# Optimization experiments

Measured on AMD Instinct MI355X. Metric: run time of the kernel, lower is better.

The kernel has to match this reference:

```python
import jax, jax.numpy as jnp
import numpy as np

EPS = 1e-5

def _ln(x):
    # LayerNorm over last dim, no affine (torch F.layer_norm default weight/bias None here)
    mu = jnp.mean(x, axis=-1, keepdims=True)
    var = jnp.var(x, axis=-1, keepdims=True)
    return (x - mu) * jax.lax.rsqrt(var + EPS)

def setup_inputs() -> dict:
    key = jax.random.key(0)
    B, S, IN, OUT = 4, 512, 256, 256
    HID = int(0.125 * IN)  # 32
    ks = jax.random.split(key, 9)
    s_in = 1.0 / np.sqrt(IN)
    s_hid = 1.0 / np.sqrt(HID)
    return {
        "x": jax.random.normal(ks[0], (B, S, IN), dtype=jnp.float32),
        # w_linear: Linear(IN->HID) then Linear(HID->IN*OUT)
        "w1": jax.random.uniform(ks[1], (HID, IN), jnp.float32, -s_in, s_in),
        "b1": jax.random.uniform(ks[2], (HID,), jnp.float32, -s_in, s_in),
        "w2": jax.random.uniform(ks[3], (IN * OUT, HID), jnp.float32, -s_hid, s_hid),
        "b2": jax.random.uniform(ks[4], (IN * OUT,), jnp.float32, -s_hid, s_hid),
        # b_linear: Linear(IN->HID) then Linear(HID->OUT)
        "u1": jax.random.uniform(ks[5], (HID, IN), jnp.float32, -s_in, s_in),
        "c1": jax.random.uniform(ks[6], (HID,), jnp.float32, -s_in, s_in),
        "u2": jax.random.uniform(ks[7], (OUT, HID), jnp.float32, -s_hid, s_hid),
        "c2": jax.random.uniform(ks[8], (OUT,), jnp.float32, -s_hid, s_hid),
    }

def reference(x, w1, b1, w2, b2, u1, c1, u2, c2):
    B, S, IN = x.shape
    OUT = u2.shape[0]
    # weight generation: [B,S,IN] -> [B,S,HID] -> [B,S,OUT*IN]
    hw = jnp.einsum('bsi,hi->bsh', x, w1) + b1
    w = jnp.einsum('bsh,oh->bso', hw, w2) + b2  # o = OUT*IN flattened
    w = w.reshape(B, S, OUT, IN)
    w = _ln(w)  # LayerNorm over IN
    # bias generation: [B,S,IN] -> [B,S,HID] -> [B,S,OUT]
    hb = jnp.einsum('bsi,hi->bsh', x, u1) + c1
    b = jnp.einsum('bsh,oh->bso', hb, u2) + c2
    b = _ln(b)  # LayerNorm over OUT
    # batched matvec: y[b,s,o] = sum_i w[b,s,o,i] * x[b,s,i] + b[b,s,o]
    y = jnp.einsum('bsoi,bsi->bso', w, x) + b
    return y
```

## Files before the change

### kernel.cpp

```cpp
#include <hip/hip_runtime.h>
#include <hip/hip_bf16.h>
#include <stdint.h>

#define EPS 1e-5f

typedef __attribute__((ext_vector_type(8))) short short8;
typedef __attribute__((ext_vector_type(4))) float f32x4;

typedef const __attribute__((address_space(1))) uint32_t gas_u32;
typedef __attribute__((address_space(3))) uint32_t las_u32;

static __device__ __forceinline__ void gll16(const void* src, void* dst) {
    __builtin_amdgcn_global_load_lds((gas_u32*)src, (las_u32*)dst, 16, 0, 0);
}
static __device__ __forceinline__ unsigned short f2b(float f) {
    __hip_bfloat16 h = __float2bfloat16(f);
    return *reinterpret_cast<unsigned short*>(&h);
}
static __device__ __forceinline__ float b2f(unsigned short u) {
    union { unsigned int i; float f; } x; x.i = ((unsigned int)u) << 16; return x.f;
}
static __device__ __forceinline__ unsigned int pk2(float a, float b) {
    return (unsigned int)f2b(a) | ((unsigned int)f2b(b) << 16);
}

__device__ void prep_body(int o, const float* __restrict__ w2,
                          const float* __restrict__ b2,
                          unsigned short* __restrict__ BW,
                          unsigned short* __restrict__ BQ,
                          float* __restrict__ qb2f, float* __restrict__ sb2f,
                          char* smem)
{
    float* w2s = (float*)smem;
    float* b2s = w2s + 8192;

    const int tid = threadIdx.x, lane = tid & 63, wave = tid >> 6;
    const float* w2o = w2 + (size_t)o * 8192;

    #pragma unroll
    for (int q = 0; q < 8; ++q) {
        int I = wave * 8 + q;
        gll16(w2o + I * 256 + lane * 4, w2s + I * 256);
    }
    if (wave == 0) gll16(b2 + (size_t)o * 256 + lane * 4, b2s);
    asm volatile("s_waitcnt vmcnt(0)" ::: "memory");
    __syncthreads();

    for (int k = 0; k < 5; ++k) {
        int u = tid + k * 256;
        if (u < 1056) {
            int r = u >> 5, s = u & 31;
            float vv[8];
            #pragma unroll
            for (int d = 0; d < 8; ++d)
                vv[d] = (r < 32) ? w2s[(s * 8 + d) * 32 + r] : b2s[s * 8 + d];
            uint4 pk;
            pk.x = pk2(vv[0], vv[1]); pk.y = pk2(vv[2], vv[3]);
            pk.z = pk2(vv[4], vv[5]); pk.w = pk2(vv[6], vv[7]);
            *(uint4*)&BW[((size_t)o * 33 + r) * 256 + s * 8] = pk;
        }
    }

    {
        const int h = tid & 31, hp0 = tid >> 5;
        float acc[4] = {0.f, 0.f, 0.f, 0.f};
        for (int i = 0; i < 256; ++i) {
            float wh = w2s[i * 32 + h];
            #pragma unroll
            for (int k = 0; k < 4; ++k)
                acc[k] += w2s[i * 32 + hp0 + 8 * k] * wh;
        }
        #pragma unroll
        for (int k = 0; k < 4; ++k)
            BQ[((size_t)o * 34 + (hp0 + 8 * k)) * 32 + h] = f2b(acc[k]);
    }

    if (tid < 32) {
        float pa = 0.f, sa = 0.f;
        for (int i = 0; i < 256; ++i) {
            float wv = w2s[i * 32 + tid];
            pa += wv * b2s[i];
            sa += wv;
        }
        BQ[((size_t)o * 34 + 32) * 32 + tid] = f2b(2.0f * pa);
        BQ[((size_t)o * 34 + 33) * 32 + tid] = f2b(sa);
    } else if (tid == 32) {
        float sb = 0.f, qb = 0.f;
        for (int i = 0; i < 256; ++i) { float bv = b2s[i]; sb += bv; qb += bv * bv; }
        sb2f[o] = sb;
        qb2f[o] = qb;
    }
}

__device__ void ka_body4(int tb, const float* __restrict__ x,
                         const float* __restrict__ w1, const float* __restrict__ b1,
                         const float* __restrict__ u1, const float* __restrict__ c1,
                         const float* __restrict__ u2, const float* __restrict__ c2,
                         unsigned short* __restrict__ xbf,
                         unsigned short* __restrict__ hwbf,
                         float* __restrict__ sxf,
                         unsigned short* __restrict__ blnbf,
                         char* smem)
{
    const int tid = threadIdx.x, l = tid & 63, wave = tid >> 6;
    const int t = tb * 4 + wave;

    float* xs = (float*)smem + wave * 288;
    float* hb = xs + 256;

    float4 x4 = reinterpret_cast<const float4*>(x + (size_t)t * 256)[l];
    reinterpret_cast<float4*>(xs)[l] = x4;

    float s = x4.x + x4.y + x4.z + x4.w;
    #pragma unroll
    for (int off = 32; off > 0; off >>= 1) s += __shfl_xor(s, off);
    if (l == 0) sxf[t] = s;

    {
        ushort4 ux;
        ux.x = f2b(x4.x); ux.y = f2b(x4.y); ux.z = f2b(x4.z); ux.w = f2b(x4.w);
        *reinterpret_cast<ushort4*>(xbf + (size_t)t * 256 + l * 4) = ux;
    }
    __syncthreads();

    const float* wrow = (l < 32) ? (w1 + (size_t)l * 256) : (u1 + (size_t)(l - 32) * 256);
    float acc = (l < 32) ? b1[l] : c1[l - 32];
    #pragma unroll 8
    for (int i = 0; i < 256; i += 4) {
        float4 w = *reinterpret_cast<const float4*>(wrow + i);
        acc += w.x * xs[i] + w.y * xs[i + 1] + w.z * xs[i + 2] + w.w * xs[i + 3];
    }
    if (l < 32) hwbf[(size_t)t * 32 + l] = f2b(acc);
    else        hb[l - 32] = acc;
    __syncthreads();

    float bv[4];
    #pragma unroll
    for (int r = 0; r < 4; ++r) {
        const int oo = l * 4 + r;
        const float* urow = u2 + (size_t)oo * 32;
        float a = c2[oo];
        #pragma unroll
        for (int h = 0; h < 32; h += 4) {
            float4 u = *reinterpret_cast<const float4*>(urow + h);
            a += u.x * hb[h] + u.y * hb[h + 1] + u.z * hb[h + 2] + u.w * hb[h + 3];
        }
        bv[r] = a;
    }
    float ss = bv[0] + bv[1] + bv[2] + bv[3];
    float qs = bv[0]*bv[0] + bv[1]*bv[1] + bv[2]*bv[2] + bv[3]*bv[3];
    #pragma unroll
    for (int off = 32; off > 0; off >>= 1) {
        ss += __shfl_xor(ss, off);
        qs += __shfl_xor(qs, off);
    }
    const float mu  = ss * (1.0f / 256.f);
    const float var = qs * (1.0f / 256.f) - mu * mu;
    const float inv = rsqrtf(var + EPS);
    #pragma unroll
    for (int r = 0; r < 4; ++r)
        blnbf[(size_t)t * 256 + l * 4 + r] = f2b((bv[r] - mu) * inv);
}

__global__ __launch_bounds__(256)
void k_pre(const float* __restrict__ x,
           const float* __restrict__ w1, const float* __restrict__ b1,
           const float* __restrict__ w2, const float* __restrict__ b2,
           const float* __restrict__ u1, const float* __restrict__ c1,
           const float* __restrict__ u2, const float* __restrict__ c2,
           unsigned short* __restrict__ BW, unsigned short* __restrict__ BQ,
           float* __restrict__ qb2f, float* __restrict__ sb2f,
           unsigned short* __restrict__ xbf, unsigned short* __restrict__ hwbf,
           float* __restrict__ sxf, unsigned short* __restrict__ blnbf)
{
    __shared__ __align__(16) char smem[33792];
    const int b = blockIdx.x;
    if (b < 256) prep_body(b, w2, b2, BW, BQ, qb2f, sb2f, smem);
    else         ka_body4(b - 256, x, w1, b1, u1, c1, u2, c2, xbf, hwbf, sxf, blnbf, smem);
}

__global__ __launch_bounds__(256, 2)
void k_main(const unsigned short* __restrict__ BW,
            const unsigned short* __restrict__ BQ,
            const unsigned short* __restrict__ xbf,
            const unsigned short* __restrict__ hwbf,
            const float* __restrict__ sxf,
            const float* __restrict__ qb2f,
            const float* __restrict__ sb2f,
            const unsigned short* __restrict__ blnbf,
            float* __restrict__ y)
{
    __shared__ __align__(16) unsigned short Ash[64 * 256];
    __shared__ __align__(16) unsigned short Bb[2][82 * 64];
    __shared__ __align__(16) unsigned short hwT[64 * 32];
    __shared__ __align__(16) unsigned short BQT[2][82 * 32];
    __shared__ float scr[3][64][2];

    const int tid = threadIdx.x, lane = tid & 63, wave = tid >> 6;
    const int c = lane & 15, g = lane >> 4;
    const int wr = wave >> 1, wc = wave & 1;
    const int b = blockIdx.x;
    const int og_grp = b & 15, tt = b >> 4;
    const int t0 = tt * 64;
    const int obase = og_grp * 16;

    {
        uint4 z = make_uint4(0, 0, 0, 0);
        { int bu = tid >> 7, j = tid & 127;
          *(uint4*)&Bb[bu][(528 + j) * 8] = z; }
        if (tid < 112) { int bu = tid / 56, j = tid % 56;
          *(uint4*)&BQT[bu][(272 + j) * 8] = z; }
    }
    {
        int u = wave * 64 + lane;
        gll16(hwbf + (size_t)(t0 + (u >> 2)) * 32 + (u & 3) * 8,
              (unsigned short*)hwT + u * 8);
    }
    #pragma unroll
    for (int k = 0; k < 8; ++k) {
        int u = wave * 512 + k * 64 + lane;
        int r = u >> 5, s = u & 31, kc = s >> 3, s8 = s & 7;
        gll16(xbf + (size_t)(t0 + r) * 256 + kc * 64 + ((s8 ^ (r & 7)) * 8),
              Ash + u * 8);
    }

    auto stageBQT = [&](int o2, int bq) {
        #pragma unroll
        for (int k = 0; k < 2; ++k) {
            int u = wave * 68 + k * 64 + lane;
            if (u < wave * 68 + 68) {
                int rr = u >> 2, s = u & 3;
                int ol = rr >= 34 ? 1 : 0, rl = rr - 34 * ol;
                gll16(BQ + ((size_t)(o2 + ol) * 34 + rl) * 32 + s * 8,
                      (unsigned short*)BQT[bq] + u * 8);
            }
        }
    };
    auto stageB = [&](int o2, int kc, int bf) {
        #pragma unroll
        for (int k = 0; k < 3; ++k) {
            int u = wave * 132 + k * 64 + lane;
            if (u < wave * 132 + 132) {
                int rr = u >> 3, s = u & 7;
                int ol = rr >= 33 ? 1 : 0, rl = rr - 33 * ol;
                gll16(BW + ((size_t)(o2 + ol) * 33 + rl) * 256 + kc * 64 + ((s ^ (rr & 7)) * 8),
                      (unsigned short*)Bb[bf] + u * 8);
            }
        }
    };

    stageBQT(obase, 0);
    stageB(obase, 0, 0);
    asm volatile("s_waitcnt vmcnt(3)" ::: "memory");
    __syncthreads();

    short8 afr[2][2][4];
    #pragma unroll
    for (int mt = 0; mt < 2; ++mt) {
        const int row = wr * 32 + mt * 16 + c;
        #pragma unroll
        for (int kc = 0; kc < 4; ++kc)
            #pragma unroll
            for (int ku = 0; ku < 2; ++ku)
                afr[mt][ku][kc] = *(const short8*)&Ash[row * 256 + kc * 64 + (((ku * 4 + g) ^ (c & 7)) * 8)];
    }
    short8 a2f[2];
    a2f[0] = *(const short8*)&hwT[(wr * 32 + c) * 32 + g * 8];
    a2f[1] = *(const short8*)&hwT[(wr * 32 + 16 + c) * 32 + g * 8];
    float hwa[2][4], hwb[2][4];
    #pragma unroll
    for (int mt = 0; mt < 2; ++mt)
        #pragma unroll
        for (int j = 0; j < 4; ++j) {
            int tl = wr * 32 + mt * 16 + g * 4 + j;
            hwa[mt][j] = b2f(hwT[tl * 32 + c]);
            hwb[mt][j] = b2f(hwT[tl * 32 + 16 + c]);
        }

    for (int og = 0; og < 8; ++og) {
        const int o2 = obase + og * 2;
        f32x4 acc1[2][3], acc2[2][3];
        #pragma unroll
        for (int mt = 0; mt < 2; ++mt)
            #pragma unroll
            for (int nb = 0; nb < 3; ++nb) {
                acc1[mt][nb] = (f32x4){0, 0, 0, 0};
                acc2[mt][nb] = (f32x4){0, 0, 0, 0};
            }

        #pragma unroll
        for (int kc = 0; kc < 4; ++kc) {
            if (kc < 3) {
                stageB(o2, kc + 1, (kc + 1) & 1);
                asm volatile("s_waitcnt vmcnt(3)" ::: "memory");
            } else if (og < 7) {
                stageB(o2 + 2, 0, 0);
                stageBQT(o2 + 2, (og + 1) & 1);
                asm volatile("s_waitcnt vmcnt(5)" ::: "memory");
            } else {
                asm volatile("s_waitcnt vmcnt(0)" ::: "memory");
            }
            __builtin_amdgcn_s_barrier();

            {
                const unsigned short* Bbuf = (const unsigned short*)Bb[kc & 1];
                short8 bb[3][2];
                #pragma unroll
                for (int nb = 0; nb < 3; ++nb) {
                    int h = nb * 16 + c;
                    int rr = (h < 33) ? (wc * 33 + h) : (66 + h - 33);
                    #pragma unroll
                    for (int ku = 0; ku < 2; ++ku)
                        bb[nb][ku] = *(const short8*)&Bbuf[rr * 64 + (((ku * 4 + g) ^ (rr & 7)) * 8)];
                }
                #pragma unroll
                for (int ku = 0; ku < 2; ++ku)
                    #pragma unroll
                    for (int mt = 0; mt < 2; ++mt)
                        #pragma unroll
                        for (int nb = 0; nb < 3; ++nb)
                            acc1[mt][nb] = __builtin_amdgcn_mfma_f32_16x16x32_bf16(
                                afr[mt][ku][kc], bb[nb][ku], acc1[mt][nb], 0, 0, 0);
            }
            __builtin_amdgcn_s_barrier();
        }

        {
            const unsigned short* Q = (const unsigned short*)BQT[og & 1];
            short8 bq[3];
            #pragma unroll
            for (int nb = 0; nb < 3; ++nb) {
                int h = nb * 16 + c;
                int rr = (h < 34) ? (wc * 34 + h) : (68 + h - 34);
                bq[nb] = *(const short8*)&Q[rr * 32 + g * 8];
            }
            #pragma unroll
            for (int mt = 0; mt < 2; ++mt)
                #pragma unroll
                for (int nb = 0; nb < 3; ++nb)
                    acc2[mt][nb] = __builtin_amdgcn_mfma_f32_16x16x32_bf16(
                        a2f[mt], bq[nb], acc2[mt][nb], 0, 0, 0);
        }

        #pragma unroll
        for (int mt = 0; mt < 2; ++mt) {
            float vdw[4], vqq[4], vsw[4];
            #pragma unroll
            for (int j = 0; j < 4; ++j) {
                vdw[j] = acc1[mt][0][j] * hwa[mt][j] + acc1[mt][1][j] * hwb[mt][j] + acc1[mt][2][j];
                float q2t = (c == 1) ? 0.0f : acc2[mt][2][j];
                vqq[j] = acc2[mt][0][j] * hwa[mt][j] + acc2[mt][1][j] * hwb[mt][j] + q2t;
                vsw[j] = acc2[mt][2][j];
            }
            #pragma unroll
            for (int off = 1; off <= 8; off <<= 1)
                #pragma unroll
                for (int j = 0; j < 4; ++j) {
                    vdw[j] += __shfl_xor(vdw[j], off);
                    vqq[j] += __shfl_xor(vqq[j], off);
                }
            #pragma unroll
            for (int j = 0; j < 4; ++j) {
                int tl = wr * 32 + mt * 16 + g * 4 + j;
                if (c == 0) { scr[0][tl][wc] = vdw[j]; scr[1][tl][wc] = vqq[j]; }
                if (c == 1) { scr[2][tl][wc] = vsw[j]; }
            }
        }
        __syncthreads();

        if (tid < 128) {
            int tl = tid >> 1, ol = tid & 1;
            int t = t0 + tl, o = o2 + ol;
            float dw = scr[0][tl][ol];
            float qq = scr[1][tl][ol] + qb2f[o];
            float sw = scr[2][tl][ol] + sb2f[o];
            float mu  = sw * (1.0f / 256.f);
            float var = qq * (1.0f / 256.f) - mu * mu;
            float inv = rsqrtf(var + EPS);
            float bl = b2f(blnbf[(size_t)t * 256 + o]);
            y[(size_t)t * 256 + o] = inv * (dw - mu * sxf[t]) + bl;
        }
        __syncthreads();
    }
}

extern "C" void kernel_launch(void* const* d_in, const int* in_sizes, int n_in,
                              void* d_out, int out_size, void* d_ws, size_t ws_size,
                              hipStream_t stream)
{
    (void)in_sizes; (void)n_in; (void)out_size; (void)ws_size;
    const float* x  = (const float*)d_in[0];
    const float* w1 = (const float*)d_in[1];
    const float* b1 = (const float*)d_in[2];
    const float* w2 = (const float*)d_in[3];
    const float* b2 = (const float*)d_in[4];
    const float* u1 = (const float*)d_in[5];
    const float* c1 = (const float*)d_in[6];
    const float* u2 = (const float*)d_in[7];
    const float* c2 = (const float*)d_in[8];
    float* y = (float*)d_out;

    char* ws = (char*)d_ws;
    unsigned short* BW    = (unsigned short*)(ws);
    unsigned short* BQ    = (unsigned short*)(ws + 4325376);
    unsigned short* xbf   = (unsigned short*)(ws + 4882432);
    unsigned short* hwbf  = (unsigned short*)(ws + 5931008);
    float*          sxf   = (float*)         (ws + 6062080);
    float*          qb2f  = (float*)         (ws + 6070272);
    float*          sb2f  = (float*)         (ws + 6071296);
    unsigned short* blnbf = (unsigned short*)(ws + 6072320);

    k_pre<<<768, 256, 0, stream>>>(x, w1, b1, w2, b2, u1, c1, u2, c2,
                                   BW, BQ, qb2f, sb2f, xbf, hwbf, sxf, blnbf);
    k_main<<<512, 256, 0, stream>>>(BW, BQ, xbf, hwbf, sxf, qb2f, sb2f, blnbf, y);
}
```

Measured before the change: 69.05 us.

## Compute weight-prep Gram matrices with bf16 MFMA on transposed swizzled LDS copy

```diff
diff --git a/kernel.cpp b/kernel.cpp
--- a/kernel.cpp
+++ b/kernel.cpp
@@ -33,8 +33,10 @@
 {
     float* w2s = (float*)smem;
     float* b2s = w2s + 8192;
+    unsigned short* mT = (unsigned short*)(b2s + 256);
 
     const int tid = threadIdx.x, lane = tid & 63, wave = tid >> 6;
+    const int c = lane & 15, g = lane >> 4;
     const float* w2o = w2 + (size_t)o * 8192;
 
     #pragma unroll
@@ -44,51 +46,89 @@
     }
     if (wave == 0) gll16(b2 + (size_t)o * 256 + lane * 4, b2s);
     asm volatile("s_waitcnt vmcnt(0)" ::: "memory");
+    __syncthreads();
+
+    {
+        const int hp = tid >> 3, oct = tid & 7;
+        float v[32];
+        #pragma unroll
+        for (int k = 0; k < 32; ++k) v[k] = w2s[(oct * 32 + k) * 32 + hp];
+        #pragma unroll
+        for (int q = 0; q < 4; ++q) {
+            uint4 pk;
+            pk.x = pk2(v[q*8+0], v[q*8+1]);
+            pk.y = pk2(v[q*8+2], v[q*8+3]);
+            pk.z = pk2(v[q*8+4], v[q*8+5]);
+            pk.w = pk2(v[q*8+6], v[q*8+7]);
+            *(uint4*)&mT[hp * 256 + (((oct*4+q) ^ (hp & 7)) * 8)] = pk;
+        }
+    }
+    if (tid < 32) {
+        uint4 ones = make_uint4(0x3F803F80u, 0x3F803F80u, 0x3F803F80u, 0x3F803F80u);
+        *(uint4*)&mT[32 * 256 + tid * 8] = ones;
+    } else if (tid < 64) {
+        int s = tid - 32;
+        uint4 pk;
+        pk.x = pk2(b2s[s*8+0], b2s[s*8+1]);
+        pk.y = pk2(b2s[s*8+2], b2s[s*8+3]);
+        pk.z = pk2(b2s[s*8+4], b2s[s*8+5]);
+        pk.w = pk2(b2s[s*8+6], b2s[s*8+7]);
+        *(uint4*)&mT[33 * 256 + ((s ^ 1) * 8)] = pk;
+    }
     __syncthreads();
 
     for (int k = 0; k < 5; ++k) {
         int u = tid + k * 256;
         if (u < 1056) {
             int r = u >> 5, s = u & 31;
-            float vv[8];
-            #pragma unroll
-            for (int d = 0; d < 8; ++d)
-                vv[d] = (r < 32) ? w2s[(s * 8 + d) * 32 + r] : b2s[s * 8 + d];
-            uint4 pk;
-            pk.x = pk2(vv[0], vv[1]); pk.y = pk2(vv[2], vv[3]);
-            pk.z = pk2(vv[4], vv[5]); pk.w = pk2(vv[6], vv[7]);
-            *(uint4*)&BW[((size_t)o * 33 + r) * 256 + s * 8] = pk;
-        }
-    }
-
-    {
-        const int h = tid & 31, hp0 = tid >> 5;
-        float acc[4] = {0.f, 0.f, 0.f, 0.f};
-        for (int i = 0; i < 256; ++i) {
-            float wh = w2s[i * 32 + h];
-            #pragma unroll
-            for (int k = 0; k < 4; ++k)
-                acc[k] += w2s[i * 32 + hp0 + 8 * k] * wh;
-        }
-        #pragma unroll
-        for (int k = 0; k < 4; ++k)
-            BQ[((size_t)o * 34 + (hp0 + 8 * k)) * 32 + h] = f2b(acc[k]);
-    }
-
-    if (tid < 32) {
-        float pa = 0.f, sa = 0.f;
-        for (int i = 0; i < 256; ++i) {
-            float wv = w2s[i * 32 + tid];
-            pa += wv * b2s[i];
-            sa += wv;
-        }
-        BQ[((size_t)o * 34 + 32) * 32 + tid] = f2b(2.0f * pa);
-        BQ[((size_t)o * 34 + 33) * 32 + tid] = f2b(sa);
-    } else if (tid == 32) {
-        float sb = 0.f, qb = 0.f;
-        for (int i = 0; i < 256; ++i) { float bv = b2s[i]; sb += bv; qb += bv * bv; }
-        sb2f[o] = sb;
-        qb2f[o] = qb;
+            int sr = (r < 32) ? r : 33;
+            uint4 v = *(const uint4*)&mT[sr * 256 + ((s ^ (sr & 7)) * 8)];
+            *(uint4*)&BW[((size_t)o * 33 + r) * 256 + s * 8] = v;
+        }
+    }
+
+    auto FA = [&](int a, int kk) -> short8 {
+        int row = a * 16 + c;
+        short8 z = {0,0,0,0,0,0,0,0};
+        if (row < 34)
+            return *(const short8*)&mT[row * 256 + (((kk*4+g) ^ (row & 7)) * 8)];
+        return z;
+    };
+    auto GPAIR = [&](int a, int b) -> f32x4 {
+        f32x4 acc = {0,0,0,0};
+        #pragma unroll
+        for (int kk = 0; kk < 8; ++kk)
+            acc = __builtin_amdgcn_mfma_f32_16x16x32_bf16(FA(a,kk), FA(b,kk), acc, 0,0,0);
+        return acc;
+    };
+    auto WQ2 = [&](int a, int b, f32x4 acc) {
+        #pragma unroll
+        for (int j = 0; j < 4; ++j) {
+            unsigned short v = f2b(acc[j]);
+            int r1 = a * 16 + g * 4 + j, r2 = b * 16 + c;
+            BQ[((size_t)o * 34 + r2) * 32 + r1] = v;
+            BQ[((size_t)o * 34 + r1) * 32 + r2] = v;
+        }
+    };
+    auto WEX = [&](int a, f32x4 acc) {
+        #pragma unroll
+        for (int j = 0; j < 4; ++j) {
+            int r1 = a * 16 + g * 4 + j;
+            if (c == 0)      BQ[((size_t)o * 34 + 33) * 32 + r1] = f2b(acc[j]);
+            else if (c == 1) BQ[((size_t)o * 34 + 32) * 32 + r1] = f2b(2.0f * acc[j]);
+        }
+    };
+    if (wave == 0)      WQ2(0, 0, GPAIR(0, 0));
+    else if (wave == 1) WQ2(0, 1, GPAIR(0, 1));
+    else if (wave == 2) WQ2(1, 1, GPAIR(1, 1));
+    else {
+        WEX(0, GPAIR(0, 2));
+        WEX(1, GPAIR(1, 2));
+        f32x4 a22 = GPAIR(2, 2);
+        if (g == 0 && c == 1) {
+            sb2f[o] = a22[0];
+            qb2f[o] = a22[1];
+        }
     }
 }
 
@@ -173,7 +213,7 @@
            unsigned short* __restrict__ xbf, unsigned short* __restrict__ hwbf,
            float* __restrict__ sxf, unsigned short* __restrict__ blnbf)
 {
-    __shared__ __align__(16) char smem[33792];
+    __shared__ __align__(16) char smem[51200];
     const int b = blockIdx.x;
     if (b < 256) prep_body(b, w2, b2, BW, BQ, qb2f, sb2f, smem);
     else         ka_body4(b - 256, x, w1, b1, u1, c1, u2, c2, xbf, hwbf, sxf, blnbf, smem);
```

After: 67.88 us. About the same (-1.7%).
